# Kernel optimization log

Hardware: AMD Instinct MI355X
Metric: run time of the kernel (lower is better)

Reference implementation:

```python
import jax, jax.numpy as jnp
import numpy as np

B, S, D, H = 4, 2048, 1024, 16
HD = D // H  # head_dim = 64


def setup_inputs() -> dict:
    key = jax.random.key(0)
    ks = jax.random.split(key, 6)
    sd = 1.0 / np.sqrt(D)
    return {
        "x": jax.random.normal(ks[0], (B, S, D), dtype=jnp.float32),
        "y": jax.random.normal(ks[1], (B, S, D), dtype=jnp.float32),
        "mask": jax.random.normal(ks[2], (1, 1, S, S), dtype=jnp.float32),
        "Wkv": jax.random.normal(ks[3], (D, 2 * D), dtype=jnp.float32) * sd,
        "bkv": jnp.zeros((2 * D,), dtype=jnp.float32),
        "Wq": jax.random.normal(ks[4], (D, D), dtype=jnp.float32) * sd,
        "bq": jnp.zeros((D,), dtype=jnp.float32),
        "Wo": jax.random.normal(ks[5], (D, D), dtype=jnp.float32) * sd,
        "bo": jnp.zeros((D,), dtype=jnp.float32),
    }


def reference(x, y, mask, Wkv, bkv, Wq, bq, Wo, bo):
    b, s, d = x.shape
    kv = x @ Wkv + bkv                      # [B,S,2D]
    q = y @ Wq + bq                         # [B,S,D]
    kv = kv.reshape(b, s, H, 2 * HD).transpose(0, 2, 1, 3)  # [B,H,S,2HD]
    q = q.reshape(b, s, H, HD).transpose(0, 2, 1, 3)        # [B,H,S,HD]
    k, v = kv[..., :HD], kv[..., HD:]
    scaled = jnp.einsum("bhqd,bhkd->bhqk", q, k) / jnp.sqrt(jnp.float32(HD))
    scaled = scaled + mask                  # additive mask, broadcast [1,1,S,S]
    attn = jax.nn.softmax(scaled, axis=-1)
    vals = jnp.einsum("bhqk,bhkd->bhqd", attn, v)  # [B,H,S,HD]
    vals = vals.transpose(0, 2, 1, 3).reshape(b, s, d)
    return vals @ Wo + bo
```

## Files before the change

### kernel.cpp

```cpp
#include <hip/hip_runtime.h>

#define LOG2E 1.44269504088896340736f
#define QSCALE 0.18033688011112042f

typedef __attribute__((ext_vector_type(8))) short bf16x8;
typedef __attribute__((ext_vector_type(4))) float f32x4;

__device__ __forceinline__ unsigned short f2b(float f) {
  union { float f; unsigned int u; } x; x.f = f;
  return (unsigned short)((x.u + 0x8000u) >> 16);
}

__device__ __forceinline__ unsigned int pk_bf16(float a, float b) {
  union { float f; unsigned int u; } xa, xb; xa.f = a; xb.f = b;
  return __builtin_amdgcn_perm(xb.u + 0x8000u, xa.u + 0x8000u, 0x07060302);
}

__device__ __forceinline__ void gld_lds16(const void* g, void* l) {
  __builtin_amdgcn_global_load_lds((const __attribute__((address_space(1))) void*)g,
                                   (__attribute__((address_space(3))) void*)l,
                                   16, 0, 0);
}

__device__ __forceinline__ void wgbar() {
  asm volatile("" ::: "memory");
  __builtin_amdgcn_s_barrier();
  asm volatile("" ::: "memory");
}
#define SWAIT(s) asm volatile("s_waitcnt " s ::: "memory")

__global__ __launch_bounds__(256) void cast_xy(const float* __restrict__ x,
                                               const float* __restrict__ y,
                                               unsigned short* __restrict__ xb,
                                               unsigned short* __restrict__ yb) {
  int i = blockIdx.x * 256 + threadIdx.x;
  const float* in = x; unsigned short* out = xb;
  if (i >= 2097152) { in = y; out = yb; i -= 2097152; }
  float4 v = ((const float4*)in)[i];
  uint2 o;
  o.x = pk_bf16(v.x, v.y);
  o.y = pk_bf16(v.z, v.w);
  ((uint2*)out)[i] = o;
}

__global__ __launch_bounds__(256) void scale_mask(const float* __restrict__ in,
                                                  float* __restrict__ out) {
  int i = blockIdx.x * 256 + threadIdx.x;
  f32x4 v = ((const f32x4*)in)[i];
  ((f32x4*)out)[i] = v * LOG2E;
}

__global__ __launch_bounds__(256) void transpose_cast_all(
    const float* __restrict__ Wkv, const float* __restrict__ Wq,
    const float* __restrict__ Wo, unsigned short* __restrict__ wkvt,
    unsigned short* __restrict__ wqt, unsigned short* __restrict__ wot) {
  __shared__ float t[32][33];
  int tb = blockIdx.x;
  const float* W; unsigned short* Wt; int N;
  if (tb < 2048)      { W = Wkv; Wt = wkvt; N = 2048; }
  else if (tb < 3072) { W = Wq;  Wt = wqt;  N = 1024; tb -= 2048; }
  else                { W = Wo;  Wt = wot;  N = 1024; tb -= 3072; }
  const int K = 1024;
  int tilesN = N >> 5;
  int nb = (tb % tilesN) * 32, kb = (tb / tilesN) * 32;
  int j = threadIdx.x & 31, i0 = threadIdx.x >> 5;
  #pragma unroll
  for (int p = 0; p < 4; ++p) {
    int i = i0 + p * 8;
    t[i][j] = W[(size_t)(kb + i) * N + nb + j];
  }
  __syncthreads();
  #pragma unroll
  for (int p = 0; p < 4; ++p) {
    int i = i0 + p * 8;
    Wt[(size_t)(nb + i) * K + kb + j] = f2b(t[j][i]);
  }
}

template <int MODE>
__global__ __launch_bounds__(256)
void gemm128(const unsigned short* __restrict__ A,
             const unsigned short* __restrict__ Bt,
             const float* __restrict__ bias,
             void* __restrict__ out0, void* __restrict__ out1,
             int M, int N, int K) {
  __shared__ __align__(16) unsigned short As[128 * 64];
  __shared__ __align__(16) unsigned short Bs[128 * 64];
  const int tid = threadIdx.x;
  const int bn = blockIdx.x, bm = blockIdx.y;
  const int wave = tid >> 6, lane = tid & 63;
  const int wm = (wave >> 1) * 64, wn = (wave & 1) * 64;
  const int lrow = lane & 15, quad = lane >> 4;
  const int sw = lrow & 7;

  f32x4 acc[4][4];
  #pragma unroll
  for (int i = 0; i < 4; ++i)
    #pragma unroll
    for (int j = 0; j < 4; ++j)
      #pragma unroll
      for (int r = 0; r < 4; ++r) acc[i][j][r] = 0.f;

  const unsigned short* Ab = A + (size_t)(bm * 128) * K;
  const unsigned short* Bb = Bt + (size_t)(bn * 128) * K;

  for (int k0 = 0; k0 < K; k0 += 64) {
    #pragma unroll
    for (int i = 0; i < 4; ++i) {
      int e = i * 256 + tid;
      int row = e >> 3, gs = (e & 7) ^ (row & 7);
      gld_lds16(Ab + (size_t)row * K + k0 + gs * 8, &As[e * 8]);
    }
    #pragma unroll
    for (int i = 0; i < 4; ++i) {
      int e = i * 256 + tid;
      int row = e >> 3, gs = (e & 7) ^ (row & 7);
      gld_lds16(Bb + (size_t)row * K + k0 + gs * 8, &Bs[e * 8]);
    }
    __builtin_amdgcn_s_waitcnt(0);
    __syncthreads();
    #pragma unroll
    for (int ks = 0; ks < 2; ++ks) {
      bf16x8 af[4], bf[4];
      const int g = ((ks * 4 + quad) ^ sw) * 8;
      #pragma unroll
      for (int i = 0; i < 4; ++i)
        af[i] = *(const bf16x8*)&As[(wm + i * 16 + lrow) * 64 + g];
      #pragma unroll
      for (int j = 0; j < 4; ++j)
        bf[j] = *(const bf16x8*)&Bs[(wn + j * 16 + lrow) * 64 + g];
      #pragma unroll
      for (int i = 0; i < 4; ++i)
        #pragma unroll
        for (int j = 0; j < 4; ++j)
          acc[i][j] = __builtin_amdgcn_mfma_f32_16x16x32_bf16(af[i], bf[j], acc[i][j], 0, 0, 0);
    }
    __syncthreads();
  }

  const int col0 = bn * 128 + wn;
  #pragma unroll
  for (int i = 0; i < 4; ++i) {
    const int row0 = bm * 128 + wm + i * 16 + quad * 4;
    const int b = row0 >> 11, s0 = row0 & 2047;
    #pragma unroll
    for (int j = 0; j < 4; ++j) {
      const int cc = j * 16 + lrow;
      const float bv = bias[col0 + cc];
      float v0 = acc[i][j][0] + bv, v1 = acc[i][j][1] + bv;
      float v2 = acc[i][j][2] + bv, v3 = acc[i][j][3] + bv;
      if (MODE == 0) {
        float* C = (float*)out0;
        size_t off = (size_t)row0 * N + col0 + cc;
        C[off] = v0; C[off + N] = v1; C[off + 2 * N] = v2; C[off + 3 * N] = v3;
      } else if (MODE == 1) {
        const int h = col0 >> 7;
        if ((col0 & 64) == 0) {
          unsigned short* Kb = (unsigned short*)out0;
          size_t base = ((size_t)(b * 16 + h) * 2048 + s0) * 64 + cc;
          Kb[base] = f2b(v0); Kb[base + 64] = f2b(v1);
          Kb[base + 128] = f2b(v2); Kb[base + 192] = f2b(v3);
        } else {
          unsigned short* Vt = (unsigned short*)out1;
          size_t base = ((size_t)(b * 16 + h) * 64 + cc) * 2048 + s0;
          uint2 p; p.x = pk_bf16(v0, v1); p.y = pk_bf16(v2, v3);
          *(uint2*)&Vt[base] = p;
        }
      } else {
        v0 *= QSCALE; v1 *= QSCALE; v2 *= QSCALE; v3 *= QSCALE;
        const int h = col0 >> 6;
        unsigned short* Qb = (unsigned short*)out0;
        size_t base = ((size_t)(b * 16 + h) * 2048 + s0) * 64 + cc;
        Qb[base] = f2b(v0); Qb[base + 64] = f2b(v1);
        Qb[base + 128] = f2b(v2); Qb[base + 192] = f2b(v3);
      }
    }
  }
}


#define ATTN_TILE(t, ZC, ZN)                                                   \
  {                                                                            \
    unsigned short* Kc = &Ks[(t) & 1][0];                                      \
    unsigned short* Kn = &Ks[((t) + 1) & 1][0];                                \
    unsigned short* Vc = &Vs[(t) & 1][0];                                      \
    unsigned short* Vn = &Vs[((t) + 1) & 1][0];                                \
    const int ktn = ((t) + 1) & 31;        \
    SWAIT("vmcnt(0)");      \
    wgbar();                   \
    _Pragma("unroll")                                                          \
    for (int i = 0; i < 2; ++i) {                            \
      int e = i * 256 + tid;                                                   \
      int row = e >> 3, gs = (e & 7) ^ (row & 7);                              \
      gld_lds16(kp + (size_t)(ktn * 64 + row) * 64 + gs * 8, &Kn[e * 8]);      \
    }                                                                          \
    _Pragma("unroll")                                                          \
    for (int i = 0; i < 2; ++i) {                            \
      int e = i * 256 + tid;                                                   \
      int row = e >> 3, gs = (e & 7) ^ (row & 7);                              \
      gld_lds16(vp + (size_t)row * 2048 + ktn * 64 + gs * 8, &Vn[e * 8]);      \
    }                                                                          \
    _Pragma("unroll")                                                          \
    for (int iq = 0; iq < 2; ++iq) {                    \
      const float* mrow =                                                      \
          mp + (size_t)(iq * 16 + lrow) * 2048 + quad * 4 + ktn * 64;          \
      ZN[0][iq] = *(const f32x4*)(mrow);                                       \
      ZN[1][iq] = *(const f32x4*)(mrow + 16);                                  \
      ZN[2][iq] = *(const f32x4*)(mrow + 32);                                  \
      ZN[3][iq] = *(const f32x4*)(mrow + 48);                                  \
    }                                                                          \
    _Pragma("unroll")                                                          \
    for (int ik = 0; ik < 4; ++ik) {               \
      const int krow = (ik * 16 + lrow) * 64;                                  \
      bf16x8 kf0 = *(const bf16x8*)&Kc[krow + ((quad ^ sw) * 8)];              \
      bf16x8 kf1 = *(const bf16x8*)&Kc[krow + (((4 + quad) ^ sw) * 8)];        \
      _Pragma("unroll")                                                        \
      for (int iq = 0; iq < 2; ++iq) {                                         \
        f32x4 zz = ZC[ik][iq];                                                 \
        zz = __builtin_amdgcn_mfma_f32_16x16x32_bf16(kf0, qf[iq][0], zz, 0, 0, 0); \
        zz = __builtin_amdgcn_mfma_f32_16x16x32_bf16(kf1, qf[iq][1], zz, 0, 0, 0); \
        float e0 = exp2f(zz[0]), e1 = exp2f(zz[1]);                            \
        float e2 = exp2f(zz[2]), e3 = exp2f(zz[3]);                            \
        lsum[iq] += (e0 + e1) + (e2 + e3);                                     \
        uint2 p;                                                               \
        p.x = pk_bf16(e0, e1);                                                 \
        p.y = pk_bf16(e2, e3);                                                 \
        *(uint2*)&Ps[(w * 32 + iq * 16 + lrow) * 64 +                          \
                     ((ik * 2 + (quad >> 1)) ^ sw) * 8 + (quad & 1) * 4] = p;  \
      }                                                                        \
    }                                                                          \
    SWAIT("lgkmcnt(0)");          \
    _Pragma("unroll")                                                          \
    for (int ks = 0; ks < 2; ++ks) {                       \
      bf16x8 vf[4], pf[2];                                                     \
      const int g = ((ks * 4 + quad) ^ sw) * 8;                                \
      _Pragma("unroll")                                                        \
      for (int id = 0; id < 4; ++id)                                           \
        vf[id] = *(const bf16x8*)&Vc[(id * 16 + lrow) * 64 + g];               \
      _Pragma("unroll")                                                        \
      for (int iq = 0; iq < 2; ++iq)                                           \
        pf[iq] = *(const bf16x8*)&Ps[(w * 32 + iq * 16 + lrow) * 64 + g];      \
      _Pragma("unroll")                                                        \
      for (int id = 0; id < 4; ++id)                                           \
        _Pragma("unroll")                                                      \
        for (int iq = 0; iq < 2; ++iq)                                         \
          o_acc[id][iq] = __builtin_amdgcn_mfma_f32_16x16x32_bf16(             \
              vf[id], pf[iq], o_acc[id][iq], 0, 0, 0);                         \
    }                                                                          \
  }

__global__ __launch_bounds__(256, 3)
void attn(const unsigned short* __restrict__ Qbuf,
          const unsigned short* __restrict__ Kbuf,
          const unsigned short* __restrict__ Vtbuf,
          const float* __restrict__ masks,
          unsigned short* __restrict__ vals) {
  const int blk = blockIdx.x;
  const int xcd = blk & 7, slot = blk >> 3;
  const int qt = xcd * 2 + (slot >> 6);
  const int hb = slot & 63;
  const int b = hb >> 4, h = hb & 15;
  const int tid = threadIdx.x, lane = tid & 63, w = tid >> 6;
  const int lrow = lane & 15, quad = lane >> 4;
  const int sw = lrow & 7;

  __shared__ __align__(16) unsigned short Ks[2][64 * 64];
  __shared__ __align__(16) unsigned short Vs[2][64 * 64];
  __shared__ __align__(16) unsigned short Ps[128 * 64];

  const unsigned short* qp = Qbuf + ((size_t)(b * 16 + h) * 2048 + qt * 128) * 64;
  const unsigned short* kp = Kbuf + (size_t)(b * 16 + h) * 2048 * 64;
  const unsigned short* vp = Vtbuf + (size_t)(b * 16 + h) * 64 * 2048;
  const float* mp = masks + (size_t)(qt * 128 + w * 32) * 2048;

  #pragma unroll
  for (int i = 0; i < 4; ++i) {
    int e = i * 256 + tid;
    int row = e >> 3, gs = (e & 7) ^ (row & 7);
    gld_lds16(qp + (size_t)row * 64 + gs * 8, &Ps[e * 8]);
  }
  #pragma unroll
  for (int i = 0; i < 2; ++i) {
    int e = i * 256 + tid;
    int row = e >> 3, gs = (e & 7) ^ (row & 7);
    gld_lds16(kp + (size_t)row * 64 + gs * 8, &Ks[0][e * 8]);
  }
  #pragma unroll
  for (int i = 0; i < 2; ++i) {
    int e = i * 256 + tid;
    int row = e >> 3, gs = (e & 7) ^ (row & 7);
    gld_lds16(vp + (size_t)row * 2048 + gs * 8, &Vs[0][e * 8]);
  }
  f32x4 zm0[4][2], zm1[4][2];
  #pragma unroll
  for (int iq = 0; iq < 2; ++iq) {
    const float* mrow = mp + (size_t)(iq * 16 + lrow) * 2048 + quad * 4;
    zm0[0][iq] = *(const f32x4*)(mrow);
    zm0[1][iq] = *(const f32x4*)(mrow + 16);
    zm0[2][iq] = *(const f32x4*)(mrow + 32);
    zm0[3][iq] = *(const f32x4*)(mrow + 48);
  }
  SWAIT("vmcnt(0)");
  wgbar();

  bf16x8 qf[2][2];
  #pragma unroll
  for (int iq = 0; iq < 2; ++iq)
    #pragma unroll
    for (int ks = 0; ks < 2; ++ks)
      qf[iq][ks] = *(const bf16x8*)&Ps[(w * 32 + iq * 16 + lrow) * 64 + ((ks * 4 + quad) ^ sw) * 8];

  f32x4 o_acc[4][2];
  #pragma unroll
  for (int id = 0; id < 4; ++id)
    #pragma unroll
    for (int iq = 0; iq < 2; ++iq)
      #pragma unroll
      for (int r = 0; r < 4; ++r) o_acc[id][iq][r] = 0.f;
  float lsum[2] = {0.f, 0.f};

  for (int t2 = 0; t2 < 16; ++t2) {
    ATTN_TILE(2 * t2,     zm0, zm1);
    ATTN_TILE(2 * t2 + 1, zm1, zm0);
  }

  unsigned short* ob = vals + (size_t)(b * 2048 + qt * 128 + w * 32) * 1024 + h * 64;
  #pragma unroll
  for (int iq = 0; iq < 2; ++iq) {
    float s = lsum[iq];
    s += __shfl_xor(s, 16);
    s += __shfl_xor(s, 32);
    float inv = 1.f / s;
    #pragma unroll
    for (int id = 0; id < 4; ++id) {
      uint2 p;
      p.x = pk_bf16(o_acc[id][iq][0] * inv, o_acc[id][iq][1] * inv);
      p.y = pk_bf16(o_acc[id][iq][2] * inv, o_acc[id][iq][3] * inv);
      *(uint2*)&ob[(size_t)(iq * 16 + lrow) * 1024 + id * 16 + quad * 4] = p;
    }
  }
}

extern "C" void kernel_launch(void* const* d_in, const int* in_sizes, int n_in,
                              void* d_out, int out_size, void* d_ws, size_t ws_size,
                              hipStream_t stream) {
  const float* x    = (const float*)d_in[0];
  const float* y    = (const float*)d_in[1];
  const float* mask = (const float*)d_in[2];
  const float* Wkv  = (const float*)d_in[3];
  const float* bkv  = (const float*)d_in[4];
  const float* Wq   = (const float*)d_in[5];
  const float* bq   = (const float*)d_in[6];
  const float* Wo   = (const float*)d_in[7];
  const float* bo   = (const float*)d_in[8];

  char* ws = (char*)d_ws;
  unsigned short* xb    = (unsigned short*)(ws + ((size_t)0 << 20));
  unsigned short* yb    = (unsigned short*)(ws + ((size_t)16 << 20));
  unsigned short* wkvt  = (unsigned short*)(ws + ((size_t)32 << 20));
  unsigned short* wqt   = (unsigned short*)(ws + ((size_t)36 << 20));
  unsigned short* wot   = (unsigned short*)(ws + ((size_t)38 << 20));
  unsigned short* kbuf  = (unsigned short*)(ws + ((size_t)40 << 20));
  unsigned short* vtbuf = (unsigned short*)(ws + ((size_t)56 << 20));
  unsigned short* qbuf  = (unsigned short*)(ws + ((size_t)72 << 20));
  unsigned short* valsb = (unsigned short*)(ws + ((size_t)88 << 20));
  float*          masks = (float*)        (ws + ((size_t)108 << 20));

  cast_xy<<<16384, 256, 0, stream>>>(x, y, xb, yb);
  scale_mask<<<4096, 256, 0, stream>>>(mask, masks);
  transpose_cast_all<<<4096, 256, 0, stream>>>(Wkv, Wq, Wo, wkvt, wqt, wot);

  gemm128<1><<<dim3(16, 64), 256, 0, stream>>>(xb, wkvt, bkv, kbuf, vtbuf, 8192, 2048, 1024);
  gemm128<2><<<dim3(8, 64), 256, 0, stream>>>(yb, wqt, bq, qbuf, nullptr, 8192, 1024, 1024);
  attn<<<1024, 256, 0, stream>>>(qbuf, kbuf, vtbuf, masks, valsb);
  gemm128<0><<<dim3(8, 64), 256, 0, stream>>>(valsb, wot, bo, (float*)d_out, nullptr, 8192, 1024, 1024);
}
```

Before: 456.3 us.

## Fold mask scaling into attention, split tile into halves to raise occupancy

Removes the separate scale_mask kernel and multiplies the raw mask by LOG2E inside the attention kernel. Each K/V tile is processed in two halves with a half-width P buffer in LDS, and mask prefetch is split into two register sets so fewer registers stay live. This allows launch bounds of 4 blocks per SM instead of 3. Q fragments are now loaded straight from global memory into registers rather than staged through LDS. The barrier waits only for the K/V loads (vmcnt(4)) rather than draining everything, which adds risk if the counter does not match the issued loads.

```diff
diff --git a/kernel.cpp b/kernel.cpp
--- a/kernel.cpp
+++ b/kernel.cpp
@@ -28,6 +28,7 @@
   asm volatile("" ::: "memory");
 }
 #define SWAIT(s) asm volatile("s_waitcnt " s ::: "memory")
+#define FENCE    asm volatile("" ::: "memory")
 
 __global__ __launch_bounds__(256) void cast_xy(const float* __restrict__ x,
                                                const float* __restrict__ y,
@@ -41,13 +42,6 @@
   o.x = pk_bf16(v.x, v.y);
   o.y = pk_bf16(v.z, v.w);
   ((uint2*)out)[i] = o;
-}
-
-__global__ __launch_bounds__(256) void scale_mask(const float* __restrict__ in,
-                                                  float* __restrict__ out) {
-  int i = blockIdx.x * 256 + threadIdx.x;
-  f32x4 v = ((const f32x4*)in)[i];
-  ((f32x4*)out)[i] = v * LOG2E;
 }
 
 __global__ __launch_bounds__(256) void transpose_cast_all(
@@ -179,15 +173,70 @@
 }
 
 
-#define ATTN_TILE(t, ZC, ZN)                                                   \
+#define ATTN_HALF(KS_, IK0, MH)                                                \
+  {                                                                            \
+    bf16x8 kf[2][2];                                                           \
+    _Pragma("unroll")                                                          \
+    for (int ii = 0; ii < 2; ++ii) {                                           \
+      const int krow = ((IK0 + ii) * 16 + lrow) * 64;                          \
+      kf[ii][0] = *(const bf16x8*)&Kc[krow + ((quad ^ sw) * 8)];               \
+      kf[ii][1] = *(const bf16x8*)&Kc[krow + (((4 + quad) ^ sw) * 8)];         \
+    }                                                                          \
+    _Pragma("unroll")                                                          \
+    for (int ii = 0; ii < 2; ++ii)                                             \
+      _Pragma("unroll")                                                        \
+      for (int iq = 0; iq < 2; ++iq) {                                         \
+        f32x4 zz = MH[ii][iq] * LOG2E;                                         \
+        zz = __builtin_amdgcn_mfma_f32_16x16x32_bf16(kf[ii][0], qf[iq][0], zz, 0, 0, 0); \
+        zz = __builtin_amdgcn_mfma_f32_16x16x32_bf16(kf[ii][1], qf[iq][1], zz, 0, 0, 0); \
+        float e0 = exp2f(zz[0]), e1 = exp2f(zz[1]);                            \
+        float e2 = exp2f(zz[2]), e3 = exp2f(zz[3]);                            \
+        lsum[iq] += (e0 + e1) + (e2 + e3);                                     \
+        uint2 pp; pp.x = pk_bf16(e0, e1); pp.y = pk_bf16(e2, e3);              \
+        const int rr = iq * 16 + lrow;                                         \
+        *(uint2*)&Ph[w * 1024 + rr * 32 +                                      \
+                     (((ii * 2 + (quad >> 1)) ^ ((rr >> 1) & 3)) * 8) +        \
+                     (quad & 1) * 4] = pp;                                     \
+      }                                                                        \
+    SWAIT("lgkmcnt(0)");          \
+    {                                                                          \
+      bf16x8 vf[4], pf[2];                                                     \
+      const int g = (((KS_)*4 + quad) ^ sw) * 8;                               \
+      _Pragma("unroll")                                                        \
+      for (int id = 0; id < 4; ++id)                                           \
+        vf[id] = *(const bf16x8*)&Vc[(id * 16 + lrow) * 64 + g];               \
+      _Pragma("unroll")                                                        \
+      for (int iq = 0; iq < 2; ++iq) {                                         \
+        const int rr = iq * 16 + lrow;                                         \
+        pf[iq] = *(const bf16x8*)&Ph[w * 1024 + rr * 32 +                      \
+                                     ((quad ^ ((rr >> 1) & 3)) * 8)];          \
+      }                                                                        \
+      _Pragma("unroll")                                                        \
+      for (int id = 0; id < 4; ++id)                                           \
+        _Pragma("unroll")                                                      \
+        for (int iq = 0; iq < 2; ++iq)                                         \
+          o_acc[id][iq] = __builtin_amdgcn_mfma_f32_16x16x32_bf16(             \
+              vf[id], pf[iq], o_acc[id][iq], 0, 0, 0);                         \
+    }                                                                          \
+  }
+
+#define ATTN_TILE(t)                                                           \
   {                                                                            \
     unsigned short* Kc = &Ks[(t) & 1][0];                                      \
     unsigned short* Kn = &Ks[((t) + 1) & 1][0];                                \
     unsigned short* Vc = &Vs[(t) & 1][0];                                      \
     unsigned short* Vn = &Vs[((t) + 1) & 1][0];                                \
     const int ktn = ((t) + 1) & 31;        \
-    SWAIT("vmcnt(0)");      \
-    wgbar();                   \
+    SWAIT("vmcnt(4)");   \
+    wgbar();             \
+    _Pragma("unroll")                                                          \
+    for (int iq = 0; iq < 2; ++iq) {                   \
+      const float* mr =                                                        \
+          mp + (size_t)(iq * 16 + lrow) * 2048 + (t) * 64 + quad * 4;          \
+      mh23[0][iq] = *(const f32x4*)(mr + 32);                                  \
+      mh23[1][iq] = *(const f32x4*)(mr + 48);                                  \
+    }                                                                          \
+    FENCE;                                                                     \
     _Pragma("unroll")                                                          \
     for (int i = 0; i < 2; ++i) {                            \
       int e = i * 256 + tid;                                                   \
@@ -200,60 +249,24 @@
       int row = e >> 3, gs = (e & 7) ^ (row & 7);                              \
       gld_lds16(vp + (size_t)row * 2048 + ktn * 64 + gs * 8, &Vn[e * 8]);      \
     }                                                                          \
-    _Pragma("unroll")                                                          \
-    for (int iq = 0; iq < 2; ++iq) {                    \
-      const float* mrow =                                                      \
-          mp + (size_t)(iq * 16 + lrow) * 2048 + quad * 4 + ktn * 64;          \
-      ZN[0][iq] = *(const f32x4*)(mrow);                                       \
-      ZN[1][iq] = *(const f32x4*)(mrow + 16);                                  \
-      ZN[2][iq] = *(const f32x4*)(mrow + 32);                                  \
-      ZN[3][iq] = *(const f32x4*)(mrow + 48);                                  \
-    }                                                                          \
-    _Pragma("unroll")                                                          \
-    for (int ik = 0; ik < 4; ++ik) {               \
-      const int krow = (ik * 16 + lrow) * 64;                                  \
-      bf16x8 kf0 = *(const bf16x8*)&Kc[krow + ((quad ^ sw) * 8)];              \
-      bf16x8 kf1 = *(const bf16x8*)&Kc[krow + (((4 + quad) ^ sw) * 8)];        \
-      _Pragma("unroll")                                                        \
-      for (int iq = 0; iq < 2; ++iq) {                                         \
-        f32x4 zz = ZC[ik][iq];                                                 \
-        zz = __builtin_amdgcn_mfma_f32_16x16x32_bf16(kf0, qf[iq][0], zz, 0, 0, 0); \
-        zz = __builtin_amdgcn_mfma_f32_16x16x32_bf16(kf1, qf[iq][1], zz, 0, 0, 0); \
-        float e0 = exp2f(zz[0]), e1 = exp2f(zz[1]);                            \
-        float e2 = exp2f(zz[2]), e3 = exp2f(zz[3]);                            \
-        lsum[iq] += (e0 + e1) + (e2 + e3);                                     \
-        uint2 p;                                                               \
-        p.x = pk_bf16(e0, e1);                                                 \
-        p.y = pk_bf16(e2, e3);                                                 \
-        *(uint2*)&Ps[(w * 32 + iq * 16 + lrow) * 64 +                          \
-                     ((ik * 2 + (quad >> 1)) ^ sw) * 8 + (quad & 1) * 4] = p;  \
-      }                                                                        \
-    }                                                                          \
-    SWAIT("lgkmcnt(0)");          \
-    _Pragma("unroll")                                                          \
-    for (int ks = 0; ks < 2; ++ks) {                       \
-      bf16x8 vf[4], pf[2];                                                     \
-      const int g = ((ks * 4 + quad) ^ sw) * 8;                                \
-      _Pragma("unroll")                                                        \
-      for (int id = 0; id < 4; ++id)                                           \
-        vf[id] = *(const bf16x8*)&Vc[(id * 16 + lrow) * 64 + g];               \
-      _Pragma("unroll")                                                        \
-      for (int iq = 0; iq < 2; ++iq)                                           \
-        pf[iq] = *(const bf16x8*)&Ps[(w * 32 + iq * 16 + lrow) * 64 + g];      \
-      _Pragma("unroll")                                                        \
-      for (int id = 0; id < 4; ++id)                                           \
-        _Pragma("unroll")                                                      \
-        for (int iq = 0; iq < 2; ++iq)                                         \
-          o_acc[id][iq] = __builtin_amdgcn_mfma_f32_16x16x32_bf16(             \
-              vf[id], pf[iq], o_acc[id][iq], 0, 0, 0);                         \
-    }                                                                          \
-  }
-
-__global__ __launch_bounds__(256, 3)
+    FENCE;                                                                     \
+    ATTN_HALF(0, 0, mh01)                                                      \
+    ATTN_HALF(1, 2, mh23)                                                      \
+    FENCE;                                                                     \
+    _Pragma("unroll")                                                          \
+    for (int iq = 0; iq < 2; ++iq) {                 \
+      const float* mr =                                                        \
+          mp + (size_t)(iq * 16 + lrow) * 2048 + ktn * 64 + quad * 4;          \
+      mh01[0][iq] = *(const f32x4*)(mr);                                       \
+      mh01[1][iq] = *(const f32x4*)(mr + 16);                                  \
+    }                                                                          \
+  }
+
+__global__ __launch_bounds__(256, 4)
 void attn(const unsigned short* __restrict__ Qbuf,
           const unsigned short* __restrict__ Kbuf,
           const unsigned short* __restrict__ Vtbuf,
-          const float* __restrict__ masks,
+          const float* __restrict__ mask,
           unsigned short* __restrict__ vals) {
   const int blk = blockIdx.x;
   const int xcd = blk & 7, slot = blk >> 3;
@@ -266,19 +279,21 @@
 
   __shared__ __align__(16) unsigned short Ks[2][64 * 64];
   __shared__ __align__(16) unsigned short Vs[2][64 * 64];
-  __shared__ __align__(16) unsigned short Ps[128 * 64];
+  __shared__ __align__(16) unsigned short Ph[4 * 1024];
 
   const unsigned short* qp = Qbuf + ((size_t)(b * 16 + h) * 2048 + qt * 128) * 64;
   const unsigned short* kp = Kbuf + (size_t)(b * 16 + h) * 2048 * 64;
   const unsigned short* vp = Vtbuf + (size_t)(b * 16 + h) * 64 * 2048;
-  const float* mp = masks + (size_t)(qt * 128 + w * 32) * 2048;
-
-  #pragma unroll
-  for (int i = 0; i < 4; ++i) {
-    int e = i * 256 + tid;
-    int row = e >> 3, gs = (e & 7) ^ (row & 7);
-    gld_lds16(qp + (size_t)row * 64 + gs * 8, &Ps[e * 8]);
-  }
+  const float* mp = mask + (size_t)(qt * 128 + w * 32) * 2048;
+
+  bf16x8 qf[2][2];
+  #pragma unroll
+  for (int iq = 0; iq < 2; ++iq)
+    #pragma unroll
+    for (int ks = 0; ks < 2; ++ks)
+      qf[iq][ks] = *(const bf16x8*)(qp + (size_t)(w * 32 + iq * 16 + lrow) * 64 +
+                                    ks * 32 + quad * 8);
+  FENCE;
   #pragma unroll
   for (int i = 0; i < 2; ++i) {
     int e = i * 256 + tid;
@@ -291,24 +306,14 @@
     int row = e >> 3, gs = (e & 7) ^ (row & 7);
     gld_lds16(vp + (size_t)row * 2048 + gs * 8, &Vs[0][e * 8]);
   }
-  f32x4 zm0[4][2], zm1[4][2];
+  FENCE;
+  f32x4 mh01[2][2], mh23[2][2];
   #pragma unroll
   for (int iq = 0; iq < 2; ++iq) {
-    const float* mrow = mp + (size_t)(iq * 16 + lrow) * 2048 + quad * 4;
-    zm0[0][iq] = *(const f32x4*)(mrow);
-    zm0[1][iq] = *(const f32x4*)(mrow + 16);
-    zm0[2][iq] = *(const f32x4*)(mrow + 32);
-    zm0[3][iq] = *(const f32x4*)(mrow + 48);
-  }
-  SWAIT("vmcnt(0)");
-  wgbar();
-
-  bf16x8 qf[2][2];
-  #pragma unroll
-  for (int iq = 0; iq < 2; ++iq)
-    #pragma unroll
-    for (int ks = 0; ks < 2; ++ks)
-      qf[iq][ks] = *(const bf16x8*)&Ps[(w * 32 + iq * 16 + lrow) * 64 + ((ks * 4 + quad) ^ sw) * 8];
+    const float* mr = mp + (size_t)(iq * 16 + lrow) * 2048 + quad * 4;
+    mh01[0][iq] = *(const f32x4*)(mr);
+    mh01[1][iq] = *(const f32x4*)(mr + 16);
+  }
 
   f32x4 o_acc[4][2];
   #pragma unroll
@@ -320,8 +325,8 @@
   float lsum[2] = {0.f, 0.f};
 
   for (int t2 = 0; t2 < 16; ++t2) {
-    ATTN_TILE(2 * t2,     zm0, zm1);
-    ATTN_TILE(2 * t2 + 1, zm1, zm0);
+    ATTN_TILE(2 * t2);
+    ATTN_TILE(2 * t2 + 1);
   }
 
   unsigned short* ob = vals + (size_t)(b * 2048 + qt * 128 + w * 32) * 1024 + h * 64;
@@ -364,14 +369,12 @@
   unsigned short* vtbuf = (unsigned short*)(ws + ((size_t)56 << 20));
   unsigned short* qbuf  = (unsigned short*)(ws + ((size_t)72 << 20));
   unsigned short* valsb = (unsigned short*)(ws + ((size_t)88 << 20));
-  float*          masks = (float*)        (ws + ((size_t)108 << 20));
 
   cast_xy<<<16384, 256, 0, stream>>>(x, y, xb, yb);
-  scale_mask<<<4096, 256, 0, stream>>>(mask, masks);
   transpose_cast_all<<<4096, 256, 0, stream>>>(Wkv, Wq, Wo, wkvt, wqt, wot);
 
   gemm128<1><<<dim3(16, 64), 256, 0, stream>>>(xb, wkvt, bkv, kbuf, vtbuf, 8192, 2048, 1024);
   gemm128<2><<<dim3(8, 64), 256, 0, stream>>>(yb, wqt, bq, qbuf, nullptr, 8192, 1024, 1024);
-  attn<<<1024, 256, 0, stream>>>(qbuf, kbuf, vtbuf, masks, valsb);
+  attn<<<1024, 256, 0, stream>>>(qbuf, kbuf, vtbuf, mask, valsb);
   gemm128<0><<<dim3(8, 64), 256, 0, stream>>>(valsb, wot, bo, (float*)d_out, nullptr, 8192, 1024, 1024);
 }
```

Result: slower. 496.0 us (+8.7%).
